# Kernel optimization log

Measured on AMD Instinct MI355X. Metric: run time of the kernel, lower is better.

The kernel has to match this reference:

```python
import jax, jax.numpy as jnp
import numpy as np

E = 8        # number of sessions (experts)
N = 512      # per-session input width (max units)
P = 512      # n_channels (output width)
F = 100      # max_F time bins
B = 128      # batch of trials
SCALE = 1.0


def setup_inputs() -> dict:
    key = jax.random.key(0)
    kx, ke, k1, k2, k3, k4 = jax.random.split(key, 6)
    x = jax.random.normal(kx, (B, F, N), dtype=jnp.float32)
    eid = jax.random.randint(ke, (B,), 0, E, dtype=jnp.int32)
    # Per-session stitcher Linear(N, 2N) and projector Linear(2N, P), stacked.
    s1 = 1.0 / np.sqrt(N)
    s2 = 1.0 / np.sqrt(2 * N)
    W1 = jax.random.uniform(k1, (E, N, 2 * N), jnp.float32, -s1, s1)
    b1 = jax.random.uniform(k2, (E, 2 * N), jnp.float32, -s1, s1)
    W2 = jax.random.uniform(k3, (E, 2 * N, P), jnp.float32, -s2, s2)
    b2 = jax.random.uniform(k4, (E, P), jnp.float32, -s2, s2)
    return {"x": x, "eid": eid, "W1": W1, "b1": b1, "W2": W2, "b2": b2}


def reference(x, eid, W1, b1, W2, b2):
    # Grouped (per-session) Linear -> Softsign -> Linear, dispatched by eid.
    # Equivalent to the torch loop over unique eids with mask gather/scatter,
    # expressed as a gather of per-sample expert weights + batched matmul.
    w1 = W1[eid]                      # [B, N, 2N]
    stitched = jnp.einsum('bfn,bnh->bfh', x, w1) + b1[eid][:, None, :]
    act = stitched / (1.0 + jnp.abs(stitched))  # Softsign
    act = act * SCALE
    w2 = W2[eid]                      # [B, 2N, P]
    out = jnp.einsum('bfh,bhp->bfp', act, w2) + b2[eid][:, None, :]
    return out                        # [B, F, P]
```

## Files before the change

### kernel.cpp

```cpp
#include <hip/hip_runtime.h>
#include <hip/hip_bf16.h>

#define B_ 128
#define F_ 100
#define N_ 512
#define H_ 1024
#define P_ 512
#define E_ 8
#define BK 64

typedef __attribute__((ext_vector_type(8))) short bf16x8;
typedef __attribute__((ext_vector_type(4))) float f32x4;

#define GLOAD16(g, l) __builtin_amdgcn_global_load_lds(                      \
    (const __attribute__((address_space(1))) void*)(g),                      \
    (__attribute__((address_space(3))) void*)(l), 16, 0, 0)

static __device__ __forceinline__ short f2bf(float f) {
    __hip_bfloat16 h = __float2bfloat16(f);
    short s;
    __builtin_memcpy(&s, &h, sizeof(s));
    return s;
}

__global__ __launch_bounds__(256) void prep(
    const float* __restrict__ x, const float* __restrict__ W1,
    const float* __restrict__ W2, const int* __restrict__ eid,
    short* __restrict__ xbf, short* __restrict__ W1T, short* __restrict__ W2T,
    int2* __restrict__ ttab) {
    __shared__ float tile[64][65];
    __shared__ int scnt[E_], sbase[E_];
    const int bx = blockIdx.x;
    const int t = threadIdx.x;
    if (bx < 3200) {
        const int g = bx * 256 + t;
        const int col = (g & 63) * 8;
        const int row = g >> 6;
        const float* xp = x + (size_t)row * N_ + col;
        const float4 v0 = *(const float4*)(xp);
        const float4 v1 = *(const float4*)(xp + 4);
        union { short s[8]; uint4 u; } o;
        o.s[0] = f2bf(v0.x); o.s[1] = f2bf(v0.y);
        o.s[2] = f2bf(v0.z); o.s[3] = f2bf(v0.w);
        o.s[4] = f2bf(v1.x); o.s[5] = f2bf(v1.y);
        o.s[6] = f2bf(v1.z); o.s[7] = f2bf(v1.w);
        *(uint4*)(xbf + (size_t)row * N_ + col) = o.u;
    } else if (bx < 5248) {
        const float* W; short* WT; int R, C, r0, c0, e;
        if (bx < 4224) {
            const int idx = bx - 3200;
            e = idx >> 7; const int i = idx & 127;
            W = W1; WT = W1T; R = N_; C = H_;
            r0 = (i >> 4) * 64; c0 = (i & 15) * 64;
        } else {
            const int idx = bx - 4224;
            e = idx >> 7; const int i = idx & 127;
            W = W2; WT = W2T; R = H_; C = P_;
            r0 = (i & 15) * 64; c0 = (i >> 4) * 64;
        }
        const float* Wp = W + (size_t)e * R * C;
        short* WTp = WT + (size_t)e * C * R;
        {
            const int c4 = (t & 15) * 4, r = t >> 4;
#pragma unroll
            for (int p = 0; p < 4; p++) {
                const int row = p * 16 + r;
                const float4 v = *(const float4*)(Wp + (size_t)(r0 + row) * C + c0 + c4);
                tile[row][c4 + 0] = v.x; tile[row][c4 + 1] = v.y;
                tile[row][c4 + 2] = v.z; tile[row][c4 + 3] = v.w;
            }
        }
        __syncthreads();
        {
            const int r8 = (t & 7) * 8, cl = t >> 3;
#pragma unroll
            for (int p = 0; p < 2; p++) {
                const int c = p * 32 + cl;
                union { short s[8]; uint4 u; } o;
#pragma unroll
                for (int j = 0; j < 8; j++) o.s[j] = f2bf(tile[r8 + j][c]);
                *(uint4*)(&WTp[(size_t)(c0 + c) * R + r0 + r8]) = o.u;
            }
        }
    } else {
        if (t < E_) scnt[t] = 0;
        __syncthreads();
        int my_e = 0;
        if (t < B_) { my_e = eid[t]; atomicAdd(&scnt[my_e], 1); }
        __syncthreads();
        if (t == 0) {
            int s = 0;
            for (int i = 0; i < E_; i++) { sbase[i] = s; s += scnt[i]; }
        }
        __syncthreads();
        if (t < B_) {
            const int pos = atomicAdd(&sbase[my_e], 1);
            ttab[pos] = make_int2(t, my_e);
        }
    }
}

template <int KDIM, int BN_, bool FIRST>
__global__ __launch_bounds__(256, 4) void gemm_kernel(
    const short* __restrict__ A,
    const short* __restrict__ WT,
    const float* __restrict__ bias,
    const int2* __restrict__ ttab,
    short* __restrict__ actout,
    float* __restrict__ out)
{
    constexpr int NCOLS = FIRST ? H_ : P_;
    constexpr int NI = BN_ / 32;
    constexpr int STAGE_SH = 128 * BK + BN_ * BK;
    constexpr int EPI_SH = 4 * 4096;
    constexpr int SBUF_SH = STAGE_SH > EPI_SH ? STAGE_SH : EPI_SH;
    __shared__ short sbuf[SBUF_SH];
    short* sA = sbuf;
    short* sB = sbuf + 128 * BK;
    const int slot = (blockIdx.x & 7) * 16 + (blockIdx.x >> 3);
    const int2 te = ttab[slot];
    const int trial = te.x, e = te.y;
    const int n0 = blockIdx.y * BN_;
    const int t = threadIdx.x;
    const int lane = t & 63, w = t >> 6;
    const int wm = (w >> 1) * 64, wn = (w & 1) * (BN_ / 2);
    const int l15 = lane & 15, quad = lane >> 4;
    const int lr = lane >> 3;
    const int lc = (((lane & 7) ^ lr) * 8);

    f32x4 acc[4][NI];
#pragma unroll
    for (int mi = 0; mi < 4; mi++)
#pragma unroll
        for (int ni = 0; ni < NI; ni++)
            acc[mi][ni] = (f32x4)(0.0f);

    float bv[NI];
#pragma unroll
    for (int ni = 0; ni < NI; ni++)
        bv[ni] = bias[(size_t)e * NCOLS + n0 + wn + ni * 16 + l15];

    const short* Ap = A + (size_t)trial * F_ * KDIM;
    const short* Bp = WT + ((size_t)e * NCOLS + n0) * KDIM;

    for (int k0 = 0; k0 < KDIM; k0 += BK) {
#pragma unroll
        for (int i = 0; i < 4; i++) {
            const int rb = w * 32 + i * 8;
            if (rb < 112)
                GLOAD16(Ap + (size_t)(rb + lr) * KDIM + k0 + lc, &sA[rb * BK]);
        }
#pragma unroll
        for (int i = 0; i < NI; i++) {
            const int rb = w * (BN_ / 4) + i * 8;
            GLOAD16(Bp + (size_t)(rb + lr) * KDIM + k0 + lc, &sB[rb * BK]);
        }
        __syncthreads();
#pragma unroll
        for (int ks = 0; ks < 2; ks++) {
            const int sw = (((ks * 4 + quad) ^ (l15 & 7)) * 8);
            bf16x8 af[4], bfr[NI];
#pragma unroll
            for (int ni = 0; ni < NI; ni++)
                bfr[ni] = *(const bf16x8*)(&sB[(wn + ni * 16 + l15) * BK + sw]);
#pragma unroll
            for (int mi = 0; mi < 4; mi++) {
                if (wm + mi * 16 < F_) {
                    af[mi] = *(const bf16x8*)(&sA[(wm + mi * 16 + l15) * BK + sw]);
#pragma unroll
                    for (int ni = 0; ni < NI; ni++)
                        acc[mi][ni] = __builtin_amdgcn_mfma_f32_16x16x32_bf16(af[mi], bfr[ni], acc[mi][ni], 0, 0, 0);
                }
            }
        }
        __syncthreads();
    }

    if constexpr (FIRST) {
        short* sW = sbuf + w * 4096;
#pragma unroll
        for (int mi = 0; mi < 4; mi++) {
#pragma unroll
            for (int ni = 0; ni < 4; ni++) {
                const int cl = ni * 16 + l15;
#pragma unroll
                for (int r = 0; r < 4; r++) {
                    const int rl = mi * 16 + quad * 4 + r;
                    float v = acc[mi][ni][r] + bv[ni];
                    v = v / (1.0f + fabsf(v));
                    sW[rl * 64 + (((cl >> 3) ^ (rl & 7)) * 8) + (cl & 7)] = f2bf(v);
                }
            }
        }
#pragma unroll
        for (int i = 0; i < 8; i++) {
            const int rl = i * 8 + lr;
            const int c = lane & 7;
            const bf16x8 v = *(const bf16x8*)(&sW[rl * 64 + ((c ^ lr) * 8)]);
            const int grow = wm + rl;
            if (grow < F_)
                *(bf16x8*)(&actout[((size_t)trial * F_ + grow) * H_ + n0 + wn + c * 8]) = v;
        }
    } else {
        float* fW = (float*)(sbuf) + w * 2048;
#pragma unroll
        for (int mi = 0; mi < 4; mi++) {
#pragma unroll
            for (int ni = 0; ni < NI; ni++) {
                const int cl = ni * 16 + l15;
#pragma unroll
                for (int r = 0; r < 4; r++) {
                    const int rl = mi * 16 + quad * 4 + r;
                    fW[rl * 32 + (((cl >> 2) ^ (rl & 7)) * 4) + (cl & 3)] =
                        acc[mi][ni][r] + bv[ni];
                }
            }
        }
#pragma unroll
        for (int i = 0; i < 8; i++) {
            const int rl = i * 8 + lr;
            const int c = lane & 7;
            const float4 v = *(const float4*)(&fW[rl * 32 + ((c ^ lr) * 4)]);
            const int grow = wm + rl;
            if (grow < F_)
                *(float4*)(&out[((size_t)trial * F_ + grow) * P_ + n0 + wn + c * 4]) = v;
        }
    }
}

extern "C" void kernel_launch(void* const* d_in, const int* in_sizes, int n_in,
                              void* d_out, int out_size, void* d_ws, size_t ws_size,
                              hipStream_t stream) {
    const float* x  = (const float*)d_in[0];
    const int* eid  = (const int*)d_in[1];
    const float* W1 = (const float*)d_in[2];
    const float* b1 = (const float*)d_in[3];
    const float* W2 = (const float*)d_in[4];
    const float* b2 = (const float*)d_in[5];
    float* out = (float*)d_out;

    char* ws = (char*)d_ws;
    short* W1T = (short*)(ws);
    short* W2T = (short*)(ws + (size_t)(8u << 20));
    short* act = (short*)(ws + (size_t)(16u << 20));
    short* xbf = (short*)(ws + (size_t)(43u << 20));
    int2* ttab = (int2*)(ws + (size_t)(57u << 20));

    prep<<<dim3(5249), 256, 0, stream>>>(x, W1, W2, eid, xbf, W1T, W2T, ttab);
    gemm_kernel<N_, 128, true><<<dim3(B_, H_ / 128), 256, 0, stream>>>(xbf, W1T, b1, ttab, act, nullptr);
    gemm_kernel<H_, 64, false><<<dim3(B_, P_ / 64), 256, 0, stream>>>(act, W2T, b2, ttab, nullptr, out);
}
```

Baseline: 155.8 us.

## Double-buffer LDS in second GEMM and widen its N tile to 128

Splits the GEMM K-loop into stage/compute helpers and adds a double-buffered LDS path so the next K tile's global-to-LDS loads overlap the current tile's MFMAs. The second GEMM uses it with BN widened from 64 to 128 and launch bounds lowered to 2 waves per SIMD. The A staging region shrinks to the 112 rows actually loaded, and the epilogue writes output in two-column-group passes so the wider tile fits the existing scratch layout. This trades fewer, larger blocks and lower occupancy for more reuse of the A tile and hidden load latency.

```diff
diff --git a/kernel.cpp b/kernel.cpp
--- a/kernel.cpp
+++ b/kernel.cpp
@@ -8,6 +8,7 @@
 #define P_ 512
 #define E_ 8
 #define BK 64
+#define AROWS 112
 
 typedef __attribute__((ext_vector_type(8))) short bf16x8;
 typedef __attribute__((ext_vector_type(4))) float f32x4;
@@ -100,8 +101,8 @@
     }
 }
 
-template <int KDIM, int BN_, bool FIRST>
-__global__ __launch_bounds__(256, 4) void gemm_kernel(
+template <int KDIM, int BN_, bool FIRST, int MINW, bool DBUF>
+__global__ __launch_bounds__(256, MINW) void gemm_kernel(
     const short* __restrict__ A,
     const short* __restrict__ WT,
     const float* __restrict__ bias,
@@ -111,12 +112,11 @@
 {
     constexpr int NCOLS = FIRST ? H_ : P_;
     constexpr int NI = BN_ / 32;
-    constexpr int STAGE_SH = 128 * BK + BN_ * BK;
+    constexpr int STAGE1 = (AROWS + BN_) * BK;
+    constexpr int NBUF = DBUF ? 2 : 1;
     constexpr int EPI_SH = 4 * 4096;
-    constexpr int SBUF_SH = STAGE_SH > EPI_SH ? STAGE_SH : EPI_SH;
+    constexpr int SBUF_SH = (STAGE1 * NBUF > EPI_SH) ? STAGE1 * NBUF : EPI_SH;
     __shared__ short sbuf[SBUF_SH];
-    short* sA = sbuf;
-    short* sB = sbuf + 128 * BK;
     const int slot = (blockIdx.x & 7) * 16 + (blockIdx.x >> 3);
     const int2 te = ttab[slot];
     const int trial = te.x, e = te.y;
@@ -143,11 +143,13 @@
     const short* Ap = A + (size_t)trial * F_ * KDIM;
     const short* Bp = WT + ((size_t)e * NCOLS + n0) * KDIM;
 
-    for (int k0 = 0; k0 < KDIM; k0 += BK) {
+    auto stage = [&](int k0, short* sbase) {
+        short* sA = sbase;
+        short* sB = sbase + AROWS * BK;
 #pragma unroll
         for (int i = 0; i < 4; i++) {
             const int rb = w * 32 + i * 8;
-            if (rb < 112)
+            if (rb < AROWS)
                 GLOAD16(Ap + (size_t)(rb + lr) * KDIM + k0 + lc, &sA[rb * BK]);
         }
 #pragma unroll
@@ -155,25 +157,50 @@
             const int rb = w * (BN_ / 4) + i * 8;
             GLOAD16(Bp + (size_t)(rb + lr) * KDIM + k0 + lc, &sB[rb * BK]);
         }
-        __syncthreads();
+    };
+
+    auto compute = [&](const short* sbase) {
+        const short* sA = sbase;
+        const short* sB = sbase + AROWS * BK;
 #pragma unroll
         for (int ks = 0; ks < 2; ks++) {
             const int sw = (((ks * 4 + quad) ^ (l15 & 7)) * 8);
-            bf16x8 af[4], bfr[NI];
+            bf16x8 af, bfr[NI];
 #pragma unroll
             for (int ni = 0; ni < NI; ni++)
                 bfr[ni] = *(const bf16x8*)(&sB[(wn + ni * 16 + l15) * BK + sw]);
 #pragma unroll
             for (int mi = 0; mi < 4; mi++) {
                 if (wm + mi * 16 < F_) {
-                    af[mi] = *(const bf16x8*)(&sA[(wm + mi * 16 + l15) * BK + sw]);
+                    af = *(const bf16x8*)(&sA[(wm + mi * 16 + l15) * BK + sw]);
 #pragma unroll
                     for (int ni = 0; ni < NI; ni++)
-                        acc[mi][ni] = __builtin_amdgcn_mfma_f32_16x16x32_bf16(af[mi], bfr[ni], acc[mi][ni], 0, 0, 0);
+                        acc[mi][ni] = __builtin_amdgcn_mfma_f32_16x16x32_bf16(af, bfr[ni], acc[mi][ni], 0, 0, 0);
                 }
             }
         }
-        __syncthreads();
+    };
+
+    if constexpr (DBUF) {
+        short* b0 = sbuf;
+        short* b1 = sbuf + STAGE1;
+        stage(0, b0);
+        __syncthreads();
+        for (int k0 = 0; k0 < KDIM; k0 += 2 * BK) {
+            stage(k0 + BK, b1);
+            compute(b0);
+            __syncthreads();
+            if (k0 + 2 * BK < KDIM) stage(k0 + 2 * BK, b0);
+            compute(b1);
+            __syncthreads();
+        }
+    } else {
+        for (int k0 = 0; k0 < KDIM; k0 += BK) {
+            stage(k0, sbuf);
+            __syncthreads();
+            compute(sbuf);
+            __syncthreads();
+        }
     }
 
     if constexpr (FIRST) {
@@ -204,26 +231,29 @@
     } else {
         float* fW = (float*)(sbuf) + w * 2048;
 #pragma unroll
-        for (int mi = 0; mi < 4; mi++) {
-#pragma unroll
-            for (int ni = 0; ni < NI; ni++) {
-                const int cl = ni * 16 + l15;
-#pragma unroll
-                for (int r = 0; r < 4; r++) {
-                    const int rl = mi * 16 + quad * 4 + r;
-                    fW[rl * 32 + (((cl >> 2) ^ (rl & 7)) * 4) + (cl & 3)] =
-                        acc[mi][ni][r] + bv[ni];
+        for (int pass = 0; pass < NI; pass += 2) {
+#pragma unroll
+            for (int mi = 0; mi < 4; mi++) {
+#pragma unroll
+                for (int nj = 0; nj < 2; nj++) {
+                    const int cl = nj * 16 + l15;
+#pragma unroll
+                    for (int r = 0; r < 4; r++) {
+                        const int rl = mi * 16 + quad * 4 + r;
+                        fW[rl * 32 + (((cl >> 2) ^ (rl & 7)) * 4) + (cl & 3)] =
+                            acc[mi][pass + nj][r] + bv[pass + nj];
+                    }
                 }
             }
-        }
-#pragma unroll
-        for (int i = 0; i < 8; i++) {
-            const int rl = i * 8 + lr;
-            const int c = lane & 7;
-            const float4 v = *(const float4*)(&fW[rl * 32 + ((c ^ lr) * 4)]);
-            const int grow = wm + rl;
-            if (grow < F_)
-                *(float4*)(&out[((size_t)trial * F_ + grow) * P_ + n0 + wn + c * 4]) = v;
+#pragma unroll
+            for (int i = 0; i < 8; i++) {
+                const int rl = i * 8 + lr;
+                const int c = lane & 7;
+                const float4 v = *(const float4*)(&fW[rl * 32 + ((c ^ lr) * 4)]);
+                const int grow = wm + rl;
+                if (grow < F_)
+                    *(float4*)(&out[((size_t)trial * F_ + grow) * P_ + n0 + wn + pass * 16 + c * 4]) = v;
+            }
         }
     }
 }
@@ -247,6 +277,6 @@
     int2* ttab = (int2*)(ws + (size_t)(57u << 20));
 
     prep<<<dim3(5249), 256, 0, stream>>>(x, W1, W2, eid, xbf, W1T, W2T, ttab);
-    gemm_kernel<N_, 128, true><<<dim3(B_, H_ / 128), 256, 0, stream>>>(xbf, W1T, b1, ttab, act, nullptr);
-    gemm_kernel<H_, 64, false><<<dim3(B_, P_ / 64), 256, 0, stream>>>(act, W2T, b2, ttab, nullptr, out);
-}
+    gemm_kernel<N_, 128, true, 4, false><<<dim3(B_, H_ / 128), 256, 0, stream>>>(xbf, W1T, b1, ttab, act, nullptr);
+    gemm_kernel<H_, 128, false, 2, true><<<dim3(B_, P_ / 128), 256, 0, stream>>>(act, W2T, b2, ttab, nullptr, out);
+}
```

Result: faster. 152.5 us (-2.1%).
